# Kernel tuning notes

Hardware: AMD Instinct MI355X
Metric: run time of the kernel (lower is better)

Reference implementation:

```python
import jax, jax.numpy as jnp
import numpy as np

N, E, D, C, NEG_SLOPE = 50000, 800000, 128, 40, 0.2


def setup_inputs() -> dict:
    key = jax.random.key(0)
    ks = jax.random.split(key, 20)
    inp = {
        'x': jax.random.normal(ks[0], (N, D), dtype=jnp.float32),
        'edge_index': jax.random.randint(ks[1], (2, E), 0, N, dtype=jnp.int64),
    }
    s = 1.0 / np.sqrt(D)
    for l in range(3):
        inp[f'W{l}'] = jax.random.normal(ks[2 + 4 * l], (D, D), dtype=jnp.float32) * s
        inp[f'a_src{l}'] = jax.random.normal(ks[3 + 4 * l], (D,), dtype=jnp.float32) * s
        inp[f'a_dst{l}'] = jax.random.normal(ks[4 + 4 * l], (D,), dtype=jnp.float32) * s
        inp[f'b{l}'] = jnp.zeros((D,), dtype=jnp.float32)
    inp['W_head'] = jax.random.normal(ks[14], (D, C), dtype=jnp.float32) * s
    inp['b_head'] = jnp.zeros((C,), dtype=jnp.float32)
    return inp


def gat_layer(x, src, dst, W, a_src, a_dst, b):
    # x: [N, D]; src/dst: [E+N] (self-loops included)
    h = x @ W                                   # [N, D] node transform
    e_s = h @ a_src                             # [N] source attention logits
    e_d = h @ a_dst                             # [N] dest attention logits
    alpha = jax.nn.leaky_relu(e_s[src] + e_d[dst], NEG_SLOPE)  # [E+N]
    # segment softmax over incoming edges of each dst node
    m = jax.ops.segment_max(alpha, dst, num_segments=N)
    ex = jnp.exp(alpha - m[dst])
    z = jax.ops.segment_sum(ex, dst, num_segments=N)
    w = ex / z[dst]                             # [E+N] normalized attention
    out = jax.ops.segment_sum(w[:, None] * h[src], dst, num_segments=N)
    return out + b


def reference(x, edge_index, W0, a_src0, a_dst0, b0, W1, a_src1, a_dst1, b1,
              W2, a_src2, a_dst2, b2, W_head, b_head):
    loops = jnp.arange(N, dtype=edge_index.dtype)
    src = jnp.concatenate([edge_index[0], loops])  # PyG add_self_loops=True
    dst = jnp.concatenate([edge_index[1], loops])
    for W, a_s, a_d, b in ((W0, a_src0, a_dst0, b0),
                           (W1, a_src1, a_dst1, b1),
                           (W2, a_src2, a_dst2, b2)):
        x = jax.nn.relu(gat_layer(x, src, dst, W, a_s, a_d, b))
        # dropout is identity in eval mode
    return x @ W_head + b_head
```

## Files before the change

kernel.cpp:

```cpp
#include <hip/hip_runtime.h>
#include <hip/hip_bf16.h>

#define NN 50000
#define EE 800000
#define DD 128
#define CC 40
#define NEG 0.2f
#define NPAD 50048
#define NB 782
#define CEDGES 2048
#define NSCAT 391
#define PADCAP 2048
#define DEGCAP 64

typedef _Float16 half8 __attribute__((ext_vector_type(8)));
typedef unsigned short ushort8 __attribute__((ext_vector_type(8)));
typedef float floatx4 __attribute__((ext_vector_type(4)));

__device__ __forceinline__ float lrelu(float a) { return a > 0.f ? a : NEG * a; }
__device__ __forceinline__ float bf2f(unsigned short u) {
    union { unsigned int i; float f; } v; v.i = (unsigned int)u << 16; return v.f;
}

__device__ __forceinline__ int edge_at(const void* ei, int i64, long long idx) {
    return i64 ? (int)((const long long*)ei)[idx] : ((const int*)ei)[idx];
}

struct ParamCvt {
    const void* src[11];
    int off[11];
    int total;
};

__global__ __launch_bounds__(256) void prep_kernel(ParamCvt a,
                                                   const void* __restrict__ x_raw,
                                                   const void* __restrict__ ei,
                                                   const void* __restrict__ W0,
                                                   const void* __restrict__ W1,
                                                   const void* __restrict__ W2,
                                                   int* __restrict__ flags,
                                                   int* __restrict__ cursor,
                                                   unsigned int* __restrict__ pairs,
                                                   float* __restrict__ params,
                                                   _Float16* __restrict__ wpack) {
    __shared__ int cnt[NB];
    __shared__ int loff[NB];
    __shared__ int gbase[NB];
    __shared__ unsigned int lp[CEDGES];
    __shared__ int wsum[4];
    __shared__ int carry;
    int t = threadIdx.x, lane = t & 63, wid = t >> 6;
    if (blockIdx.x < NSCAT) {
        unsigned int hi0 = ((const unsigned int*)ei)[2 * lane + 1];
        int i64 = (__ballot(hi0 != 0u) == 0ull) ? 1 : 0;
        for (int i = t; i < NB; i += 256) cnt[i] = 0;
        if (t == 0) carry = 0;
        __syncthreads();
        int base = blockIdx.x * CEDGES;
        int sreg[8], dreg[8];
        #pragma unroll
        for (int j = 0; j < 8; ++j) {
            int e = base + j * 256 + t;
            if (e < EE) {
                sreg[j] = edge_at(ei, i64, e);
                dreg[j] = edge_at(ei, i64, (long long)EE + e);
                atomicAdd(&cnt[dreg[j] >> 6], 1);
            } else { sreg[j] = -1; dreg[j] = -1; }
        }
        __syncthreads();
        for (int c0 = 0; c0 < NB; c0 += 256) {
            int i = c0 + t;
            int v = (i < NB) ? cnt[i] : 0;
            int x = v;
            #pragma unroll
            for (int o = 1; o < 64; o <<= 1) {
                int y = __shfl_up(x, o, 64);
                if (lane >= o) x += y;
            }
            if (lane == 63) wsum[wid] = x;
            __syncthreads();
            int carr = carry;
            int woff = 0;
            for (int w = 0; w < wid; ++w) woff += wsum[w];
            if (i < NB) loff[i] = carr + woff + x - v;
            __syncthreads();
            if (t == 0) carry = carr + wsum[0] + wsum[1] + wsum[2] + wsum[3];
            __syncthreads();
        }
        for (int i = t; i < NB; i += 256) {
            int c = cnt[i];
            gbase[i] = c ? atomicAdd(&cursor[i], c) : 0;
        }
        __syncthreads();
        for (int i = t; i < NB; i += 256) cnt[i] = loff[i];
        __syncthreads();
        #pragma unroll
        for (int j = 0; j < 8; ++j) {
            if (dreg[j] >= 0) {
                int slot = atomicAdd(&cnt[dreg[j] >> 6], 1);
                lp[slot] = ((unsigned int)dreg[j] << 16) | (unsigned int)sreg[j];
            }
        }
        __syncthreads();
        int total = (EE - base < CEDGES) ? (EE - base) : CEDGES;
        for (int i = t; i < total; i += 256) {
            unsigned int pr = lp[i];
            int b = (int)(pr >> 22);
            int idx = gbase[b] + (i - loff[b]);
            if (idx < PADCAP)
                __builtin_nontemporal_store(pr, &pairs[(size_t)b * PADCAP + idx]);
        }
        return;
    }
    int cb = blockIdx.x - NSCAT;
    unsigned short u = ((const unsigned short*)x_raw)[lane * 2];
    int e = (u >> 7) & 0xFF;
    int bad = (!(e >= 96 && e <= 158) && u != 0 && u != 0x8000) ? 1 : 0;
    int bf = (__ballot(bad) == 0ull) ? 1 : 0;
    if (cb == 217) {
        unsigned int hi = ((const unsigned int*)ei)[2 * lane + 1];
        int i64 = (__ballot(hi != 0u) == 0ull) ? 1 : 0;
        if (t == 0) { flags[0] = bf; flags[1] = i64; }
        return;
    }
    if (cb < 192) {
        int i = cb * 256 + t;
        int l = i >> 14, r = i & 16383;
        int j = r & 7, ln = (r >> 3) & 63, ks = (r >> 9) & 3, c = r >> 11;
        int k = ks * 32 + (ln >> 4) * 8 + j;
        int ncol = c * 16 + (ln & 15);
        const void* W = (l == 0) ? W0 : ((l == 1) ? W1 : W2);
        float v = bf ? bf2f(((const unsigned short*)W)[k * 128 + ncol])
                     : ((const float*)W)[k * 128 + ncol];
        wpack[i] = (_Float16)v;
    } else {
        int i = (cb - 192) * 256 + t;
        if (i >= a.total) return;
        int k = 0;
        #pragma unroll
        for (int j = 1; j < 11; ++j) if (i >= a.off[j]) k = j;
        int local = i - a.off[k];
        params[i] = bf ? bf2f(((const unsigned short*)a.src[k])[local])
                       : ((const float*)a.src[k])[local];
    }
}

__device__ __forceinline__ void gemm_core(const half8 a[4], const _Float16* __restrict__ Wg,
                                          const float* __restrict__ asrc,
                                          const float* __restrict__ adst,
                                          _Float16* __restrict__ H,
                                          float* __restrict__ es, float* __restrict__ ed,
                                          int n, int rowbase, int lane) {
    int quad = lane >> 4, col = lane & 15;
    float esp[4] = {0, 0, 0, 0}, edp[4] = {0, 0, 0, 0};
    #pragma unroll
    for (int c = 0; c < 8; ++c) {
        floatx4 acc = {0.f, 0.f, 0.f, 0.f};
        #pragma unroll
        for (int ks = 0; ks < 4; ++ks) {
            half8 b = *(const half8*)&Wg[(((c * 4 + ks) * 64) + lane) * 8];
            acc = __builtin_amdgcn_mfma_f32_16x16x32_f16(a[ks], b, acc, 0, 0, 0);
        }
        float av = asrc[c * 16 + col], dv = adst[c * 16 + col];
        #pragma unroll
        for (int r = 0; r < 4; ++r) {
            int rowg = rowbase + quad * 4 + r;
            if (rowg < n) H[(size_t)rowg * 128 + c * 16 + col] = (_Float16)acc[r];
            esp[r] += acc[r] * av;
            edp[r] += acc[r] * dv;
        }
    }
    #pragma unroll
    for (int r = 0; r < 4; ++r) {
        float s = esp[r], d = edp[r];
        #pragma unroll
        for (int o = 1; o < 16; o <<= 1) {
            s += __shfl_xor(s, o, 64);
            d += __shfl_xor(d, o, 64);
        }
        int rowg = rowbase + quad * 4 + r;
        if (col == 0 && rowg < n) { es[rowg] = s; ed[rowg] = d; }
    }
}

__device__ __forceinline__ void agg_body(const _Float16* __restrict__ H,
                                         const int* __restrict__ cnt,
                                         const unsigned short* __restrict__ csr,
                                         const float* __restrict__ es,
                                         const float* __restrict__ ed,
                                         const float* __restrict__ bias,
                                         _Float16* __restrict__ xt,
                                         int n, int blk64, int t) {
    int sub = t & 15, g = t >> 4;
    int f0 = sub * 8;
    #pragma unroll 1
    for (int r = 0; r < 4; ++r) {
        int node = blk64 + r * 16 + g;
        if (node >= n) continue;
        int total = cnt[node];
        size_t beg = (size_t)node << 6;
        float edi = ed[node];
        float wself = __expf(lrelu(es[node] + edi));
        float z = wself;
        half8 hs = *(const half8*)&H[(size_t)node * 128 + f0];
        float acc[8];
        #pragma unroll
        for (int j = 0; j < 8; ++j) acc[j] = wself * (float)hs[j];
        for (int base = 0; base < total; base += 8) {
            ushort8 c8 = *(const ushort8*)&csr[beg + base];
            int sdx[8];
            #pragma unroll
            for (int d = 0; d < 8; ++d)
                sdx[d] = (base + d < total) ? (int)c8[d] : node;
            half8 h[8];
            #pragma unroll
            for (int d = 0; d < 8; ++d)
                h[d] = *(const half8*)&H[(size_t)sdx[d] * 128 + f0];
            float wd[8];
            #pragma unroll
            for (int d = 0; d < 8; ++d) {
                float ee = __expf(lrelu(es[sdx[d]] + edi));
                wd[d] = (base + d < total) ? ee : 0.f;
                z += wd[d];
            }
            #pragma unroll
            for (int d = 0; d < 8; ++d) {
                #pragma unroll
                for (int j = 0; j < 8; ++j) acc[j] += wd[d] * (float)h[d][j];
            }
        }
        float invz = 1.f / z;
        half8 o8;
        #pragma unroll
        for (int j = 0; j < 8; ++j)
            o8[j] = (_Float16)fmaxf(acc[j] * invz + bias[f0 + j], 0.f);
        *(half8*)&xt[(size_t)(r * 16 + g) * 128 + f0] = o8;
    }
}

__global__ __launch_bounds__(256) void bucketD_gemm0(const unsigned int* __restrict__ pairs,
                                                     const int* __restrict__ cursor,
                                                     int* __restrict__ cnt,
                                                     unsigned short* __restrict__ csr,
                                                     const void* __restrict__ Xraw,
                                                     const int* __restrict__ flags,
                                                     const _Float16* __restrict__ Wp,
                                                     const float* __restrict__ asrc,
                                                     const float* __restrict__ adst,
                                                     _Float16* __restrict__ H,
                                                     float* __restrict__ es,
                                                     float* __restrict__ ed, int n) {
    __shared__ unsigned short lcsr[4096];
    __shared__ int curS[64];
    int t = threadIdx.x;
    if (blockIdx.x < NB) {
        if (t < 64) curS[t] = 0;
        __syncthreads();
        int b = blockIdx.x;
        int cntb = cursor[b];
        if (cntb > PADCAP) cntb = PADCAP;
        int pbeg = b * PADCAP;
        for (int i = t; i < cntb; i += 256) {
            unsigned int pr = pairs[pbeg + i];
            int nd = (pr >> 16) & 63;
            int p = atomicAdd(&curS[nd], 1);
            if (p < DEGCAP) lcsr[nd * 64 + p] = (unsigned short)(pr & 0xFFFF);
        }
        __syncthreads();
        if (t < 64) {
            int gid = b * 64 + t;
            if (gid < NN) {
                int v = curS[t];
                cnt[gid] = v > DEGCAP ? DEGCAP : v;
            }
        }
        for (int i = t; i < 512; i += 256)
            __builtin_nontemporal_store(((const ushort8*)lcsr)[i],
                                        &((ushort8*)csr)[(size_t)b * 512 + i]);
        return;
    }
    int gb = blockIdx.x - NB;
    int w = t >> 6, lane = t & 63;
    int quad = lane >> 4, col = lane & 15;
    int rowbase = gb * 64 + w * 16;
    half8 a[4];
    int bf = flags[0];
    int row = rowbase + col;
    if (row >= n) row = n - 1;
    if (bf) {
        const unsigned short* xr = (const unsigned short*)Xraw + (size_t)row * 128 + quad * 8;
        #pragma unroll
        for (int ks = 0; ks < 4; ++ks) {
            ushort8 u = *(const ushort8*)(xr + ks * 32);
            #pragma unroll
            for (int j = 0; j < 8; ++j) a[ks][j] = (_Float16)bf2f(u[j]);
        }
    } else {
        const float* xr = (const float*)Xraw + (size_t)row * 128 + quad * 8;
        #pragma unroll
        for (int ks = 0; ks < 4; ++ks) {
            float4 f0 = *(const float4*)(xr + ks * 32);
            float4 f1 = *(const float4*)(xr + ks * 32 + 4);
            a[ks][0] = (_Float16)f0.x; a[ks][1] = (_Float16)f0.y;
            a[ks][2] = (_Float16)f0.z; a[ks][3] = (_Float16)f0.w;
            a[ks][4] = (_Float16)f1.x; a[ks][5] = (_Float16)f1.y;
            a[ks][6] = (_Float16)f1.z; a[ks][7] = (_Float16)f1.w;
        }
    }
    gemm_core(a, Wp, asrc, adst, H, es, ed, n, rowbase, lane);
}

__global__ __launch_bounds__(256) void fused_ag(const _Float16* __restrict__ Hin,
                                                const int* __restrict__ cnt,
                                                const unsigned short* __restrict__ csr,
                                                const float* __restrict__ esin,
                                                const float* __restrict__ edin,
                                                const float* __restrict__ bias,
                                                const _Float16* __restrict__ Wp,
                                                const float* __restrict__ asrc,
                                                const float* __restrict__ adst,
                                                _Float16* __restrict__ Hout,
                                                float* __restrict__ esout,
                                                float* __restrict__ edout, int n) {
    __shared__ _Float16 xt[64 * 128];
    int t = threadIdx.x;
    agg_body(Hin, cnt, csr, esin, edin, bias, xt, n, blockIdx.x * 64, t);
    __syncthreads();
    int w = t >> 6, lane = t & 63;
    int quad = lane >> 4, col = lane & 15;
    int rowbase = blockIdx.x * 64 + w * 16;
    int rl = w * 16 + col;
    half8 a[4];
    #pragma unroll
    for (int ks = 0; ks < 4; ++ks)
        a[ks] = *(const half8*)&xt[(size_t)rl * 128 + ks * 32 + quad * 8];
    gemm_core(a, Wp, asrc, adst, Hout, esout, edout, n, rowbase, lane);
}

__global__ __launch_bounds__(256) void fused_ah(const _Float16* __restrict__ Hin,
                                                const int* __restrict__ cnt,
                                                const unsigned short* __restrict__ csr,
                                                const float* __restrict__ esin,
                                                const float* __restrict__ edin,
                                                const float* __restrict__ bias,
                                                const float* __restrict__ Whf,
                                                const float* __restrict__ bhf,
                                                const int* __restrict__ flags,
                                                void* __restrict__ out, int n) {
    __shared__ _Float16 xt[64 * 128];
    __shared__ float ws[128 * 40];
    int t = threadIdx.x;
    for (int i = t; i < 1280; i += 256)
        ((float4*)ws)[i] = ((const float4*)Whf)[i];
    agg_body(Hin, cnt, csr, esin, edin, bias, xt, n, blockIdx.x * 64, t);
    __syncthreads();
    int r = t >> 2, cg = t & 3;
    int c0 = cg * 10;
    float acc[10] = {};
    #pragma unroll 4
    for (int kb = 0; kb < 16; ++kb) {
        half8 x8 = *(const half8*)&xt[(size_t)r * 128 + kb * 8];
        #pragma unroll
        for (int j8 = 0; j8 < 8; ++j8) {
            float xr = (float)x8[j8];
            int k = kb * 8 + j8;
            #pragma unroll
            for (int j = 0; j < 10; ++j) acc[j] += xr * ws[k * 40 + c0 + j];
        }
    }
    int row = blockIdx.x * 64 + r;
    if (row < n) {
        if (flags[0]) {
            __hip_bfloat16* ob = (__hip_bfloat16*)out;
            #pragma unroll
            for (int j = 0; j < 10; ++j)
                ob[row * 40 + c0 + j] = __float2bfloat16(acc[j] + bhf[c0 + j]);
        } else {
            float* of = (float*)out;
            #pragma unroll
            for (int j = 0; j < 10; ++j)
                of[row * 40 + c0 + j] = acc[j] + bhf[c0 + j];
        }
    }
}

extern "C" void kernel_launch(void* const* d_in, const int* in_sizes, int n_in,
                              void* d_out, int out_size, void* d_ws, size_t ws_size,
                              hipStream_t stream) {
    const void* x_raw = d_in[0];
    const void* ei    = d_in[1];

    char* p = (char*)d_ws;
    auto alloc = [&](size_t bytes) { void* r = (void*)p; p += (bytes + 255) & ~(size_t)255; return r; };
    int*            flags  = (int*)alloc(16);
    _Float16*       H0     = (_Float16*)alloc((size_t)NPAD * DD * 2);
    _Float16*       H1     = (_Float16*)alloc((size_t)NPAD * DD * 2);
    float*          es0    = (float*)alloc((size_t)NN * 4);
    float*          ed0    = (float*)alloc((size_t)NN * 4);
    float*          es1    = (float*)alloc((size_t)NN * 4);
    float*          ed1    = (float*)alloc((size_t)NN * 4);
    int*            cnt    = (int*)alloc((size_t)NN * 4);
    unsigned short* csr    = (unsigned short*)alloc((size_t)NB * 4096 * 2);
    unsigned int*   pairs  = (unsigned int*)alloc((size_t)NB * PADCAP * 4);
    int*            cursor = (int*)alloc((size_t)NB * 4);
    _Float16*       wpack  = (_Float16*)alloc((size_t)3 * 16384 * 2);
    float*          params = (float*)alloc((size_t)(3 * 384 + 5160) * 4);

    ParamCvt pc;
    {
        int k = 0, off = 0;
        auto add = [&](const void* s, int nel) { pc.src[k] = s; pc.off[k] = off; off += nel; ++k; };
        for (int l = 0; l < 3; ++l) {
            add(d_in[3 + 4 * l], 128);
            add(d_in[4 + 4 * l], 128);
            add(d_in[5 + 4 * l], 128);
        }
        add(d_in[14], 5120);
        add(d_in[15], 40);
        pc.total = off;
    }

    hipMemsetAsync(cursor, 0, (size_t)NB * 4, stream);
    prep_kernel<<<NSCAT + 218, 256, 0, stream>>>(pc, x_raw, ei, d_in[2], d_in[6], d_in[10],
                                                 flags, cursor, pairs, params, wpack);

    const int ngb = NPAD / 64;
    float* base0 = params;
    float* base1 = params + 384;
    float* base2 = params + 768;
    bucketD_gemm0<<<NB + ngb, 256, 0, stream>>>(pairs, cursor, cnt, csr,
                                                x_raw, flags, wpack, base0, base0 + 128,
                                                H0, es0, ed0, NN);
    fused_ag<<<ngb, 256, 0, stream>>>(H0, cnt, csr, es0, ed0, base0 + 256,
                                      wpack + 16384, base1, base1 + 128,
                                      H1, es1, ed1, NN);
    fused_ag<<<ngb, 256, 0, stream>>>(H1, cnt, csr, es1, ed1, base1 + 256,
                                      wpack + 32768, base2, base2 + 128,
                                      H0, es0, ed0, NN);
    fused_ah<<<ngb, 256, 0, stream>>>(H0, cnt, csr, es0, ed0, base2 + 256,
                                      params + 1152, params + 1152 + 5120, flags, d_out, NN);
}
```

Baseline: 272.2 us.

## Use split-fp16 MFMA for head GEMM, halve aggregation tile, prefetch CSR

The head projection moves from a scalar FMA loop over an LDS-staged fp32 weight onto MFMA 16x16x32 f16. The weight is packed in prep as an fp16 hi/lo pair so accuracy stays close to fp32. The fused aggregation kernels now handle 32 nodes per block instead of 64, which doubles the grid, and pad the LDS tile stride to 136 to avoid bank conflicts. The CSR index vector for the next chunk is also prefetched inside the neighbour loop. In exchange, half the waves sit idle during the GEMM phase, and the head path runs extra MFMAs for padded columns.

```diff
diff --git a/kernel.cpp b/kernel.cpp
--- a/kernel.cpp
+++ b/kernel.cpp
@@ -12,6 +12,7 @@
 #define NSCAT 391
 #define PADCAP 2048
 #define DEGCAP 64
+#define XSTR 136
 
 typedef _Float16 half8 __attribute__((ext_vector_type(8)));
 typedef unsigned short ushort8 __attribute__((ext_vector_type(8)));
@@ -38,6 +39,7 @@
                                                    const void* __restrict__ W0,
                                                    const void* __restrict__ W1,
                                                    const void* __restrict__ W2,
+                                                   const void* __restrict__ Wh,
                                                    int* __restrict__ flags,
                                                    int* __restrict__ cursor,
                                                    unsigned int* __restrict__ pairs,
@@ -117,7 +119,7 @@
     int e = (u >> 7) & 0xFF;
     int bad = (!(e >= 96 && e <= 158) && u != 0 && u != 0x8000) ? 1 : 0;
     int bf = (__ballot(bad) == 0ull) ? 1 : 0;
-    if (cb == 217) {
+    if (cb == 265) {
         unsigned int hi = ((const unsigned int*)ei)[2 * lane + 1];
         int i64 = (__ballot(hi != 0u) == 0ull) ? 1 : 0;
         if (t == 0) { flags[0] = bf; flags[1] = i64; }
@@ -133,8 +135,21 @@
         float v = bf ? bf2f(((const unsigned short*)W)[k * 128 + ncol])
                      : ((const float*)W)[k * 128 + ncol];
         wpack[i] = (_Float16)v;
+    } else if (cb < 240) {
+        int i = (cb - 192) * 256 + t;
+        int p = (i >= 6144) ? 1 : 0;
+        int r = i - p * 6144;
+        int j = r & 7, ln = (r >> 3) & 63, ks = (r >> 9) & 3, c = r >> 11;
+        int k = ks * 32 + (ln >> 4) * 8 + j;
+        int ncol = c * 16 + (ln & 15);
+        float wv = 0.f;
+        if (ncol < CC)
+            wv = bf ? bf2f(((const unsigned short*)Wh)[k * CC + ncol])
+                    : ((const float*)Wh)[k * CC + ncol];
+        _Float16 hi = (_Float16)wv;
+        wpack[3 * 16384 + i] = p ? (_Float16)(wv - (float)hi) : hi;
     } else {
-        int i = (cb - 192) * 256 + t;
+        int i = (cb - 240) * 256 + t;
         if (i >= a.total) return;
         int k = 0;
         #pragma unroll
@@ -190,12 +205,12 @@
                                          const float* __restrict__ ed,
                                          const float* __restrict__ bias,
                                          _Float16* __restrict__ xt,
-                                         int n, int blk64, int t) {
+                                         int n, int blk32, int t) {
     int sub = t & 15, g = t >> 4;
     int f0 = sub * 8;
     #pragma unroll 1
-    for (int r = 0; r < 4; ++r) {
-        int node = blk64 + r * 16 + g;
+    for (int r = 0; r < 2; ++r) {
+        int node = blk32 + r * 16 + g;
         if (node >= n) continue;
         int total = cnt[node];
         size_t beg = (size_t)node << 6;
@@ -206,8 +221,10 @@
         float acc[8];
         #pragma unroll
         for (int j = 0; j < 8; ++j) acc[j] = wself * (float)hs[j];
+        ushort8 c8n = *(const ushort8*)&csr[beg];
         for (int base = 0; base < total; base += 8) {
-            ushort8 c8 = *(const ushort8*)&csr[beg + base];
+            ushort8 c8 = c8n;
+            c8n = *(const ushort8*)&csr[beg + ((base + 8) & 63)];
             int sdx[8];
             #pragma unroll
             for (int d = 0; d < 8; ++d)
@@ -234,7 +251,7 @@
         #pragma unroll
         for (int j = 0; j < 8; ++j)
             o8[j] = (_Float16)fmaxf(acc[j] * invz + bias[f0 + j], 0.f);
-        *(half8*)&xt[(size_t)(r * 16 + g) * 128 + f0] = o8;
+        *(half8*)&xt[(size_t)(r * 16 + g) * XSTR + f0] = o8;
     }
 }
 
@@ -322,18 +339,19 @@
                                                 _Float16* __restrict__ Hout,
                                                 float* __restrict__ esout,
                                                 float* __restrict__ edout, int n) {
-    __shared__ _Float16 xt[64 * 128];
+    __shared__ _Float16 xt[32 * XSTR];
     int t = threadIdx.x;
-    agg_body(Hin, cnt, csr, esin, edin, bias, xt, n, blockIdx.x * 64, t);
+    agg_body(Hin, cnt, csr, esin, edin, bias, xt, n, blockIdx.x * 32, t);
     __syncthreads();
     int w = t >> 6, lane = t & 63;
+    if (w >= 2) return;
     int quad = lane >> 4, col = lane & 15;
-    int rowbase = blockIdx.x * 64 + w * 16;
+    int rowbase = blockIdx.x * 32 + w * 16;
     int rl = w * 16 + col;
     half8 a[4];
     #pragma unroll
     for (int ks = 0; ks < 4; ++ks)
-        a[ks] = *(const half8*)&xt[(size_t)rl * 128 + ks * 32 + quad * 8];
+        a[ks] = *(const half8*)&xt[(size_t)rl * XSTR + ks * 32 + quad * 8];
     gemm_core(a, Wp, asrc, adst, Hout, esout, edout, n, rowbase, lane);
 }
 
@@ -343,43 +361,55 @@
                                                 const float* __restrict__ esin,
                                                 const float* __restrict__ edin,
                                                 const float* __restrict__ bias,
-                                                const float* __restrict__ Whf,
+                                                const _Float16* __restrict__ WhP,
                                                 const float* __restrict__ bhf,
                                                 const int* __restrict__ flags,
                                                 void* __restrict__ out, int n) {
-    __shared__ _Float16 xt[64 * 128];
-    __shared__ float ws[128 * 40];
+    __shared__ _Float16 xt[32 * XSTR];
     int t = threadIdx.x;
-    for (int i = t; i < 1280; i += 256)
-        ((float4*)ws)[i] = ((const float4*)Whf)[i];
-    agg_body(Hin, cnt, csr, esin, edin, bias, xt, n, blockIdx.x * 64, t);
+    agg_body(Hin, cnt, csr, esin, edin, bias, xt, n, blockIdx.x * 32, t);
     __syncthreads();
-    int r = t >> 2, cg = t & 3;
-    int c0 = cg * 10;
-    float acc[10] = {};
-    #pragma unroll 4
-    for (int kb = 0; kb < 16; ++kb) {
-        half8 x8 = *(const half8*)&xt[(size_t)r * 128 + kb * 8];
-        #pragma unroll
-        for (int j8 = 0; j8 < 8; ++j8) {
-            float xr = (float)x8[j8];
-            int k = kb * 8 + j8;
-            #pragma unroll
-            for (int j = 0; j < 10; ++j) acc[j] += xr * ws[k * 40 + c0 + j];
-        }
-    }
-    int row = blockIdx.x * 64 + r;
-    if (row < n) {
-        if (flags[0]) {
-            __hip_bfloat16* ob = (__hip_bfloat16*)out;
-            #pragma unroll
-            for (int j = 0; j < 10; ++j)
-                ob[row * 40 + c0 + j] = __float2bfloat16(acc[j] + bhf[c0 + j]);
-        } else {
-            float* of = (float*)out;
-            #pragma unroll
-            for (int j = 0; j < 10; ++j)
-                of[row * 40 + c0 + j] = acc[j] + bhf[c0 + j];
+    int w = t >> 6, lane = t & 63;
+    if (w >= 2) return;
+    int quad = lane >> 4, col = lane & 15;
+    int rowbase = blockIdx.x * 32 + w * 16;
+    int rl = w * 16 + col;
+    half8 a[4];
+    #pragma unroll
+    for (int ks = 0; ks < 4; ++ks)
+        a[ks] = *(const half8*)&xt[(size_t)rl * XSTR + ks * 32 + quad * 8];
+    int bf = flags[0];
+    #pragma unroll
+    for (int c = 0; c < 3; ++c) {
+        floatx4 acc = {0.f, 0.f, 0.f, 0.f};
+        #pragma unroll
+        for (int ks = 0; ks < 4; ++ks) {
+            half8 b = *(const half8*)&WhP[(((c * 4 + ks) * 64) + lane) * 8];
+            acc = __builtin_amdgcn_mfma_f32_16x16x32_f16(a[ks], b, acc, 0, 0, 0);
+        }
+        #pragma unroll
+        for (int ks = 0; ks < 4; ++ks) {
+            half8 b = *(const half8*)&WhP[6144 + (((c * 4 + ks) * 64) + lane) * 8];
+            acc = __builtin_amdgcn_mfma_f32_16x16x32_f16(a[ks], b, acc, 0, 0, 0);
+        }
+        int ocol = c * 16 + col;
+        if (ocol < CC) {
+            float bv = bhf[ocol];
+            if (bf) {
+                __hip_bfloat16* ob = (__hip_bfloat16*)out;
+                #pragma unroll
+                for (int r = 0; r < 4; ++r) {
+                    int rowg = rowbase + quad * 4 + r;
+                    if (rowg < n) ob[(size_t)rowg * CC + ocol] = __float2bfloat16(acc[r] + bv);
+                }
+            } else {
+                float* of = (float*)out;
+                #pragma unroll
+                for (int r = 0; r < 4; ++r) {
+                    int rowg = rowbase + quad * 4 + r;
+                    if (rowg < n) of[(size_t)rowg * CC + ocol] = acc[r] + bv;
+                }
+            }
         }
     }
 }
@@ -403,7 +433,7 @@
     unsigned short* csr    = (unsigned short*)alloc((size_t)NB * 4096 * 2);
     unsigned int*   pairs  = (unsigned int*)alloc((size_t)NB * PADCAP * 4);
     int*            cursor = (int*)alloc((size_t)NB * 4);
-    _Float16*       wpack  = (_Float16*)alloc((size_t)3 * 16384 * 2);
+    _Float16*       wpack  = (_Float16*)alloc((size_t)(3 * 16384 + 12288) * 2);
     float*          params = (float*)alloc((size_t)(3 * 384 + 5160) * 4);
 
     ParamCvt pc;
@@ -421,22 +451,24 @@
     }
 
     hipMemsetAsync(cursor, 0, (size_t)NB * 4, stream);
-    prep_kernel<<<NSCAT + 218, 256, 0, stream>>>(pc, x_raw, ei, d_in[2], d_in[6], d_in[10],
-                                                 flags, cursor, pairs, params, wpack);
-
-    const int ngb = NPAD / 64;
+    prep_kernel<<<NSCAT + 266, 256, 0, stream>>>(pc, x_raw, ei, d_in[2], d_in[6], d_in[10],
+                                                 d_in[14], flags, cursor, pairs, params, wpack);
+
+    const int ngb64 = NPAD / 64;
+    const int ngb32 = NPAD / 32;
     float* base0 = params;
     float* base1 = params + 384;
     float* base2 = params + 768;
-    bucketD_gemm0<<<NB + ngb, 256, 0, stream>>>(pairs, cursor, cnt, csr,
-                                                x_raw, flags, wpack, base0, base0 + 128,
-                                                H0, es0, ed0, NN);
-    fused_ag<<<ngb, 256, 0, stream>>>(H0, cnt, csr, es0, ed0, base0 + 256,
-                                      wpack + 16384, base1, base1 + 128,
-                                      H1, es1, ed1, NN);
-    fused_ag<<<ngb, 256, 0, stream>>>(H1, cnt, csr, es1, ed1, base1 + 256,
-                                      wpack + 32768, base2, base2 + 128,
-                                      H0, es0, ed0, NN);
-    fused_ah<<<ngb, 256, 0, stream>>>(H0, cnt, csr, es0, ed0, base2 + 256,
-                                      params + 1152, params + 1152 + 5120, flags, d_out, NN);
-}
+    _Float16* whpack = wpack + 3 * 16384;
+    bucketD_gemm0<<<NB + ngb64, 256, 0, stream>>>(pairs, cursor, cnt, csr,
+                                                  x_raw, flags, wpack, base0, base0 + 128,
+                                                  H0, es0, ed0, NN);
+    fused_ag<<<ngb32, 256, 0, stream>>>(H0, cnt, csr, es0, ed0, base0 + 256,
+                                        wpack + 16384, base1, base1 + 128,
+                                        H1, es1, ed1, NN);
+    fused_ag<<<ngb32, 256, 0, stream>>>(H1, cnt, csr, es1, ed1, base1 + 256,
+                                        wpack + 32768, base2, base2 + 128,
+                                        H0, es0, ed0, NN);
+    fused_ah<<<ngb32, 256, 0, stream>>>(H0, cnt, csr, es0, ed0, base2 + 256,
+                                        whpack, params + 1152 + 5120, flags, d_out, NN);
+}
```

Result: faster. 259.6 us (-4.6%).
